# Kernel optimization log

Hardware: AMD Instinct MI355X
Metric: run time of the kernel (lower is better)

Reference implementation:

```python
import jax, jax.numpy as jnp
import numpy as np

B, T, H, V, O = 64, 2048, 8, 1000, 1000


def setup_inputs() -> dict:
    key = jax.random.key(0)
    ks = jax.random.split(key, 9)
    X = jax.random.randint(ks[0], (B, T), 0, V, dtype=jnp.int64)
    lengths = jax.random.randint(ks[1], (B,), 1, T + 1, dtype=jnp.int64)
    lengths = lengths.at[0].set(T)  # ensure max(lengths) == T (static output shape)
    s = 1.0 / np.sqrt(H)
    emb = jax.random.normal(ks[2], (V, H), dtype=jnp.float32)
    W_ih = jax.random.uniform(ks[3], (H, H), jnp.float32, -s, s)
    W_hh = jax.random.uniform(ks[4], (H, H), jnp.float32, -s, s)
    b_ih = jax.random.uniform(ks[5], (H,), jnp.float32, -s, s)
    b_hh = jax.random.uniform(ks[6], (H,), jnp.float32, -s, s)
    W_out = jax.random.uniform(ks[7], (O, H), jnp.float32, -s, s)
    b_out = jax.random.uniform(ks[8], (O,), jnp.float32, -s, s)
    return {"X": X, "lengths": lengths, "emb": emb, "W_ih": W_ih,
            "W_hh": W_hh, "b_ih": b_ih, "b_hh": b_hh,
            "W_out": W_out, "b_out": b_out}


def reference(X, lengths, emb, W_ih, W_hh, b_ih, b_hh, W_out, b_out):
    # Embedding gather: [B, T, H]
    x = emb[X]
    # Precompute input projection once (equivalent to per-step W_ih @ x_t)
    x_proj = jnp.einsum('bth,ih->bti', x, W_ih) + b_ih
    h0 = jnp.zeros((X.shape[0], W_hh.shape[0]), dtype=x.dtype)

    def step(h, xt):
        h = jnp.tanh(xt + h @ W_hh.T + b_hh)
        return h, h

    # scan over time: xs shape [T, B, H]
    _, hs = jax.lax.scan(step, h0, jnp.swapaxes(x_proj, 0, 1))
    out = jnp.swapaxes(hs, 0, 1)  # [B, T, H]
    # pad_packed_sequence semantics: positions >= length are zeroed before Linear
    t_idx = jnp.arange(out.shape[1])
    mask = (t_idx[None, :] < lengths[:, None]).astype(out.dtype)  # [B, T]
    out = out * mask[:, :, None]
    # Output projection: [B, T, O]
    logits = jnp.einsum('bth,oh->bto', out, W_out) + b_out
    return logits, lengths
```

## Files before the change

kernel.cpp:

```cpp
#include <hip/hip_runtime.h>
#include <cstdint>
#include <cstddef>

#define Bz 64
#define Tz 2048
#define Hz 8
#define Vz 1000
#define Oz 1000

typedef float f32x4 __attribute__((ext_vector_type(4)));

__global__ __launch_bounds__(256) void k_xproj(
    const int* __restrict__ X, const int* __restrict__ lengths,
    const float* __restrict__ emb, const float* __restrict__ W_ih,
    const float* __restrict__ b_ih, const float* __restrict__ b_hh,
    float* __restrict__ xpT, float* __restrict__ out_tail)
{
    int r = blockIdx.x * 256 + threadIdx.x;
    if (r < Bz * Tz) {
        int v = X[r];
        const float4* e4 = (const float4*)(emb + (size_t)v * Hz);
        float4 ea = e4[0], eb = e4[1];
        float res[8];
#pragma unroll
        for (int i = 0; i < 8; ++i) {
            const float* w = W_ih + i * 8;
            float a = b_ih[i] + b_hh[i];
            a = fmaf(ea.x, w[0], a); a = fmaf(ea.y, w[1], a);
            a = fmaf(ea.z, w[2], a); a = fmaf(ea.w, w[3], a);
            a = fmaf(eb.x, w[4], a); a = fmaf(eb.y, w[5], a);
            a = fmaf(eb.z, w[6], a); a = fmaf(eb.w, w[7], a);
            res[i] = a;
        }
        int b = r >> 11, t = r & 2047;
#pragma unroll
        for (int q = 0; q < 4; ++q) {
            *(float2*)(xpT + ((size_t)(b * 4 + q) * Tz + t) * 2) =
                make_float2(res[2 * q], res[2 * q + 1]);
        }
    }
    if (r < Bz) out_tail[r] = (float)lengths[r];
}

#define QROT(x, CTRL) \
    __int_as_float(__builtin_amdgcn_update_dpp(0, __float_as_int(x), (CTRL), 0xF, 0xF, true))

__device__ __forceinline__ float fast_tanh(float a) {
#if __has_builtin(__builtin_amdgcn_exp2f)
    float m = fminf(a * 2.885390081777927f, 126.0f);
    float e = __builtin_amdgcn_exp2f(m);
#else
    float m = fminf(a * 2.885390081777927f, 126.0f);
    float e = exp2f(m);
#endif
#if __has_builtin(__builtin_amdgcn_rcpf)
    return (e - 1.0f) * __builtin_amdgcn_rcpf(e + 1.0f);
#else
    return (e - 1.0f) / (e + 1.0f);
#endif
}

#define STEP(xx, yy, toff) do { \
    float p1x = QROT(h0, 0x39), p1y = QROT(h1, 0x39); \
    float p2x = QROT(h0, 0x4E), p2y = QROT(h1, 0x4E); \
    float p3x = QROT(h0, 0x93), p3y = QROT(h1, 0x93); \
    float a0 = fmaf(h0, w0[0], (xx)); \
    float a1 = fmaf(h0, w1[0], (yy)); \
    a0 = fmaf(h1,  w0[1], a0); a1 = fmaf(h1,  w1[1], a1); \
    a0 = fmaf(p1x, w0[2], a0); a1 = fmaf(p1x, w1[2], a1); \
    a0 = fmaf(p1y, w0[3], a0); a1 = fmaf(p1y, w1[3], a1); \
    a0 = fmaf(p2x, w0[4], a0); a1 = fmaf(p2x, w1[4], a1); \
    a0 = fmaf(p2y, w0[5], a0); a1 = fmaf(p2y, w1[5], a1); \
    a0 = fmaf(p3x, w0[6], a0); a1 = fmaf(p3x, w1[6], a1); \
    a0 = fmaf(p3y, w0[7], a0); a1 = fmaf(p3y, w1[7], a1); \
    h0 = fast_tanh(a0); h1 = fast_tanh(a1); \
    *(float2*)(hs_base + (size_t)(toff) * 8) = make_float2(h0, h1); \
} while (0)

__global__ __launch_bounds__(64) void k_scan(
    const float* __restrict__ xpT, const float* __restrict__ W_hh,
    float* __restrict__ hs)
{
    int lane = threadIdx.x;
    int b = blockIdx.x * 16 + (lane >> 2);
    int q = lane & 3;
    int i0 = 2 * q, i1 = 2 * q + 1;

    float w0[8], w1[8];
#pragma unroll
    for (int r = 0; r < 4; ++r) {
        int jj = ((q + r) & 3) * 2;
        w0[2 * r]     = W_hh[i0 * 8 + jj];
        w0[2 * r + 1] = W_hh[i0 * 8 + jj + 1];
        w1[2 * r]     = W_hh[i1 * 8 + jj];
        w1[2 * r + 1] = W_hh[i1 * 8 + jj + 1];
    }

    const float4* xp4 = (const float4*)(xpT + (size_t)(b * 4 + q) * Tz * 2);
    float* hs_base = hs + (size_t)b * Tz * 8 + 2 * q;

    float h0 = 0.0f, h1 = 0.0f;
    float4 c0 = xp4[0], c1 = xp4[1], c2 = xp4[2], c3 = xp4[3];

    for (int c = 0; c < Tz / 8; ++c) {
        float4 n0 = xp4[4 * c + 4], n1 = xp4[4 * c + 5];
        float4 n2 = xp4[4 * c + 6], n3 = xp4[4 * c + 7];
        int t0 = c * 8;
        STEP(c0.x, c0.y, t0 + 0); STEP(c0.z, c0.w, t0 + 1);
        STEP(c1.x, c1.y, t0 + 2); STEP(c1.z, c1.w, t0 + 3);
        STEP(c2.x, c2.y, t0 + 4); STEP(c2.z, c2.w, t0 + 5);
        STEP(c3.x, c3.y, t0 + 6); STEP(c3.z, c3.w, t0 + 7);
        c0 = n0; c1 = n1; c2 = n2; c3 = n3;
    }
}

__global__ __launch_bounds__(256) void k_out(
    const float* __restrict__ hs, const int* __restrict__ lengths,
    const float* __restrict__ W_out, const float* __restrict__ b_out,
    float* __restrict__ out)
{
    __shared__ float4 sh4[256];
    int tid = threadIdx.x;
    int r0 = blockIdx.x * 128;

    {
        int row = r0 + (tid >> 1);
        int b = row >> 11, t = row & 2047;
        float4 v = ((const float4*)hs)[(size_t)r0 * 2 + tid];
        if (t >= lengths[b]) v = make_float4(0.f, 0.f, 0.f, 0.f);
        sh4[tid] = v;
    }
    __syncthreads();

    if (tid >= Oz / 4) return;

    float w[4][8];
    float bo[4];
#pragma unroll
    for (int k = 0; k < 4; ++k) {
        const float4* wr = (const float4*)(W_out + (size_t)(tid * 4 + k) * 8);
        float4 wa = wr[0], wb = wr[1];
        w[k][0] = wa.x; w[k][1] = wa.y; w[k][2] = wa.z; w[k][3] = wa.w;
        w[k][4] = wb.x; w[k][5] = wb.y; w[k][6] = wb.z; w[k][7] = wb.w;
        bo[k] = b_out[tid * 4 + k];
    }

    for (int rr = 0; rr < 128; ++rr) {
        float4 ha = sh4[rr * 2], hb = sh4[rr * 2 + 1];
        float r[4];
#pragma unroll
        for (int k = 0; k < 4; ++k) {
            float a = bo[k];
            a = fmaf(ha.x, w[k][0], a); a = fmaf(ha.y, w[k][1], a);
            a = fmaf(ha.z, w[k][2], a); a = fmaf(ha.w, w[k][3], a);
            a = fmaf(hb.x, w[k][4], a); a = fmaf(hb.y, w[k][5], a);
            a = fmaf(hb.z, w[k][6], a); a = fmaf(hb.w, w[k][7], a);
            r[k] = a;
        }
        f32x4 acc = { r[0], r[1], r[2], r[3] };
        __builtin_nontemporal_store(
            acc, (f32x4*)(out + (size_t)(r0 + rr) * Oz) + tid);
    }
}

extern "C" void kernel_launch(void* const* d_in, const int* in_sizes, int n_in,
                              void* d_out, int out_size, void* d_ws, size_t ws_size,
                              hipStream_t stream)
{
    const int*   X       = (const int*)d_in[0];
    const int*   lengths = (const int*)d_in[1];
    const float* emb     = (const float*)d_in[2];
    const float* W_ih    = (const float*)d_in[3];
    const float* W_hh    = (const float*)d_in[4];
    const float* b_ih    = (const float*)d_in[5];
    const float* b_hh    = (const float*)d_in[6];
    const float* W_out   = (const float*)d_in[7];
    const float* b_out   = (const float*)d_in[8];

    float* out   = (float*)d_out;
    float* xpT   = (float*)d_ws;
    float* hs    = xpT + (size_t)Bz * Tz * Hz;

    float* out_tail = out + (size_t)Bz * Tz * Oz;

    k_xproj<<<(Bz * Tz + 255) / 256, 256, 0, stream>>>(X, lengths, emb, W_ih,
                                                       b_ih, b_hh, xpT, out_tail);
    k_scan<<<Bz / 16, 64, 0, stream>>>(xpT, W_hh, hs);
    k_out<<<(Bz * Tz) / 128, 256, 0, stream>>>(hs, lengths, W_out, b_out, out);
}
```

Baseline: 749.3 us.

## Fuse recurrent scan with output projection via progress-flag pipelining

Merges the scan and output-projection kernels into one persistent launch. Block 0 runs the recurrence across four waves and publishes per-wave progress counters. The other 255 blocks spin on those counters and project each 128-step chunk as soon as it is ready, so the large output write overlaps with the serial scan. It also folds the tanh exponent scale into the input projection and W_hh, and splits the FMA chain into a shallower tree to shorten the per-step dependency. The risks are spin-wait deadlock if block 0 is not scheduled, extra sync overhead, and the fused path depending on the workspace being large enough.

```diff
diff --git a/kernel.cpp b/kernel.cpp
--- a/kernel.cpp
+++ b/kernel.cpp
@@ -8,13 +8,17 @@
 #define Vz 1000
 #define Oz 1000
 
+#define SCALE 2.885390081777927f
+
 typedef float f32x4 __attribute__((ext_vector_type(4)));
+typedef float f32x2 __attribute__((ext_vector_type(2)));
 
 __global__ __launch_bounds__(256) void k_xproj(
     const int* __restrict__ X, const int* __restrict__ lengths,
     const float* __restrict__ emb, const float* __restrict__ W_ih,
     const float* __restrict__ b_ih, const float* __restrict__ b_hh,
-    float* __restrict__ xpT, float* __restrict__ out_tail)
+    float* __restrict__ xpT, float* __restrict__ out_tail,
+    int* __restrict__ prog)
 {
     int r = blockIdx.x * 256 + threadIdx.x;
     if (r < Bz * Tz) {
@@ -30,7 +34,7 @@
             a = fmaf(ea.z, w[2], a); a = fmaf(ea.w, w[3], a);
             a = fmaf(eb.x, w[4], a); a = fmaf(eb.y, w[5], a);
             a = fmaf(eb.z, w[6], a); a = fmaf(eb.w, w[7], a);
-            res[i] = a;
+            res[i] = a * SCALE;
         }
         int b = r >> 11, t = r & 2047;
 #pragma unroll
@@ -40,17 +44,17 @@
         }
     }
     if (r < Bz) out_tail[r] = (float)lengths[r];
+    if (prog != nullptr && r < 4) prog[r] = 0;
 }
 
 #define QROT(x, CTRL) \
     __int_as_float(__builtin_amdgcn_update_dpp(0, __float_as_int(x), (CTRL), 0xF, 0xF, true))
 
-__device__ __forceinline__ float fast_tanh(float a) {
+__device__ __forceinline__ float fast_tanh_pre(float m) {
+    m = fminf(m, 126.0f);
 #if __has_builtin(__builtin_amdgcn_exp2f)
-    float m = fminf(a * 2.885390081777927f, 126.0f);
     float e = __builtin_amdgcn_exp2f(m);
 #else
-    float m = fminf(a * 2.885390081777927f, 126.0f);
     float e = exp2f(m);
 #endif
 #if __has_builtin(__builtin_amdgcn_rcpf)
@@ -64,36 +68,33 @@
     float p1x = QROT(h0, 0x39), p1y = QROT(h1, 0x39); \
     float p2x = QROT(h0, 0x4E), p2y = QROT(h1, 0x4E); \
     float p3x = QROT(h0, 0x93), p3y = QROT(h1, 0x93); \
-    float a0 = fmaf(h0, w0[0], (xx)); \
-    float a1 = fmaf(h0, w1[0], (yy)); \
-    a0 = fmaf(h1,  w0[1], a0); a1 = fmaf(h1,  w1[1], a1); \
-    a0 = fmaf(p1x, w0[2], a0); a1 = fmaf(p1x, w1[2], a1); \
-    a0 = fmaf(p1y, w0[3], a0); a1 = fmaf(p1y, w1[3], a1); \
-    a0 = fmaf(p2x, w0[4], a0); a1 = fmaf(p2x, w1[4], a1); \
-    a0 = fmaf(p2y, w0[5], a0); a1 = fmaf(p2y, w1[5], a1); \
-    a0 = fmaf(p3x, w0[6], a0); a1 = fmaf(p3x, w1[6], a1); \
-    a0 = fmaf(p3y, w0[7], a0); a1 = fmaf(p3y, w1[7], a1); \
-    h0 = fast_tanh(a0); h1 = fast_tanh(a1); \
-    *(float2*)(hs_base + (size_t)(toff) * 8) = make_float2(h0, h1); \
+    float s0a = fmaf(h1, w0[1], fmaf(h0, w0[0], (xx))); \
+    float s0b = fmaf(h1, w1[1], fmaf(h0, w1[0], (yy))); \
+    float s1a = fmaf(p1y, w0[3], p1x * w0[2]); \
+    float s1b = fmaf(p1y, w1[3], p1x * w1[2]); \
+    float s2a = fmaf(p2y, w0[5], p2x * w0[4]); \
+    float s2b = fmaf(p2y, w1[5], p2x * w1[4]); \
+    float s3a = fmaf(p3y, w0[7], p3x * w0[6]); \
+    float s3b = fmaf(p3y, w1[7], p3x * w1[6]); \
+    h0 = fast_tanh_pre((s0a + s1a) + (s2a + s3a)); \
+    h1 = fast_tanh_pre((s0b + s1b) + (s2b + s3b)); \
+    f32x2 hv = { h0, h1 }; \
+    __builtin_nontemporal_store(hv, (f32x2*)(hs_base + (size_t)(toff) * 8)); \
 } while (0)
 
-__global__ __launch_bounds__(64) void k_scan(
+__device__ __forceinline__ void scan_run(
     const float* __restrict__ xpT, const float* __restrict__ W_hh,
-    float* __restrict__ hs)
-{
-    int lane = threadIdx.x;
-    int b = blockIdx.x * 16 + (lane >> 2);
-    int q = lane & 3;
+    float* __restrict__ hs, int b, int q, int* prog, int wv)
+{
     int i0 = 2 * q, i1 = 2 * q + 1;
-
     float w0[8], w1[8];
 #pragma unroll
     for (int r = 0; r < 4; ++r) {
         int jj = ((q + r) & 3) * 2;
-        w0[2 * r]     = W_hh[i0 * 8 + jj];
-        w0[2 * r + 1] = W_hh[i0 * 8 + jj + 1];
-        w1[2 * r]     = W_hh[i1 * 8 + jj];
-        w1[2 * r + 1] = W_hh[i1 * 8 + jj + 1];
+        w0[2 * r]     = W_hh[i0 * 8 + jj]     * SCALE;
+        w0[2 * r + 1] = W_hh[i0 * 8 + jj + 1] * SCALE;
+        w1[2 * r]     = W_hh[i1 * 8 + jj]     * SCALE;
+        w1[2 * r + 1] = W_hh[i1 * 8 + jj + 1] * SCALE;
     }
 
     const float4* xp4 = (const float4*)(xpT + (size_t)(b * 4 + q) * Tz * 2);
@@ -102,15 +103,98 @@
     float h0 = 0.0f, h1 = 0.0f;
     float4 c0 = xp4[0], c1 = xp4[1], c2 = xp4[2], c3 = xp4[3];
 
-    for (int c = 0; c < Tz / 8; ++c) {
-        float4 n0 = xp4[4 * c + 4], n1 = xp4[4 * c + 5];
-        float4 n2 = xp4[4 * c + 6], n3 = xp4[4 * c + 7];
-        int t0 = c * 8;
+    for (int g = 0; g < Tz / 8; ++g) {
+        float4 n0 = xp4[4 * g + 4], n1 = xp4[4 * g + 5];
+        float4 n2 = xp4[4 * g + 6], n3 = xp4[4 * g + 7];
+        int t0 = g * 8;
         STEP(c0.x, c0.y, t0 + 0); STEP(c0.z, c0.w, t0 + 1);
         STEP(c1.x, c1.y, t0 + 2); STEP(c1.z, c1.w, t0 + 3);
         STEP(c2.x, c2.y, t0 + 4); STEP(c2.z, c2.w, t0 + 5);
         STEP(c3.x, c3.y, t0 + 6); STEP(c3.z, c3.w, t0 + 7);
         c0 = n0; c1 = n1; c2 = n2; c3 = n3;
+        if (prog != nullptr && (g & 15) == 15) {
+            if ((threadIdx.x & 63) == 0)
+                __hip_atomic_store(&prog[wv], (g >> 4) + 1,
+                                   __ATOMIC_RELEASE, __HIP_MEMORY_SCOPE_AGENT);
+        }
+    }
+}
+
+__global__ __launch_bounds__(64) void k_scan(
+    const float* __restrict__ xpT, const float* __restrict__ W_hh,
+    float* __restrict__ hs)
+{
+    int lane = threadIdx.x;
+    scan_run(xpT, W_hh, hs, blockIdx.x * 16 + (lane >> 2), lane & 3, nullptr, 0);
+}
+
+__global__ __launch_bounds__(256) void k_fused(
+    const float* __restrict__ xpT, const float* __restrict__ W_hh,
+    float* __restrict__ hs, const int* __restrict__ lengths,
+    const float* __restrict__ W_out, const float* __restrict__ b_out,
+    float* __restrict__ out, int* __restrict__ prog)
+{
+    __shared__ float4 sh4[256];
+    int tid = threadIdx.x;
+
+    if (blockIdx.x == 0) {
+        int lane = tid & 63, wv = tid >> 6;
+        scan_run(xpT, W_hh, hs, wv * 16 + (lane >> 2), lane & 3, prog, wv);
+        return;
+    }
+
+    int k0 = blockIdx.x - 1;
+
+    float w[4][8], bo[4];
+    if (tid < Oz / 4) {
+#pragma unroll
+        for (int k = 0; k < 4; ++k) {
+            const float4* wr = (const float4*)(W_out + (size_t)(tid * 4 + k) * 8);
+            float4 wa = wr[0], wb = wr[1];
+            w[k][0] = wa.x; w[k][1] = wa.y; w[k][2] = wa.z; w[k][3] = wa.w;
+            w[k][4] = wb.x; w[k][5] = wb.y; w[k][6] = wb.z; w[k][7] = wb.w;
+            bo[k] = b_out[tid * 4 + k];
+        }
+    }
+
+    for (int tau = k0; tau < (Bz * Tz) / 128; tau += 255) {
+        int c = tau >> 6;
+        int b = tau & 63;
+        if (tid == 0) {
+            while (__hip_atomic_load(&prog[b >> 4], __ATOMIC_ACQUIRE,
+                                     __HIP_MEMORY_SCOPE_AGENT) <= c)
+                __builtin_amdgcn_s_sleep(8);
+        }
+        __syncthreads();
+
+        int r0 = b * Tz + c * 128;
+        {
+            int t = c * 128 + (tid >> 1);
+            float4 v = ((const float4*)hs)[(size_t)r0 * 2 + tid];
+            if (t >= lengths[b]) v = make_float4(0.f, 0.f, 0.f, 0.f);
+            sh4[tid] = v;
+        }
+        __syncthreads();
+
+        if (tid < Oz / 4) {
+            for (int rr = 0; rr < 128; ++rr) {
+                float4 ha = sh4[rr * 2], hb = sh4[rr * 2 + 1];
+                float r[4];
+#pragma unroll
+                for (int k = 0; k < 4; ++k) {
+                    float a = bo[k];
+                    a = fmaf(ha.x, w[k][0], a); a = fmaf(ha.y, w[k][1], a);
+                    a = fmaf(ha.z, w[k][2], a); a = fmaf(ha.w, w[k][3], a);
+                    a = fmaf(hb.x, w[k][4], a); a = fmaf(hb.y, w[k][5], a);
+                    a = fmaf(hb.z, w[k][6], a); a = fmaf(hb.w, w[k][7], a);
+                    r[k] = a;
+                }
+                f32x4 acc = { r[0], r[1], r[2], r[3] };
+                __builtin_nontemporal_store(
+                    acc, (f32x4*)(out + (size_t)(r0 + rr) * Oz) + tid);
+            }
+        }
+        __syncthreads();
     }
 }
 
@@ -183,8 +267,18 @@
 
     float* out_tail = out + (size_t)Bz * Tz * Oz;
 
+    size_t base = (size_t)Bz * Tz * Hz * 4 * 2;
+    bool fused = (ws_size >= base + 64);
+    int* prog = fused ? (int*)((char*)d_ws + base) : nullptr;
+
     k_xproj<<<(Bz * Tz + 255) / 256, 256, 0, stream>>>(X, lengths, emb, W_ih,
-                                                       b_ih, b_hh, xpT, out_tail);
-    k_scan<<<Bz / 16, 64, 0, stream>>>(xpT, W_hh, hs);
-    k_out<<<(Bz * Tz) / 128, 256, 0, stream>>>(hs, lengths, W_out, b_out, out);
-}
+                                                       b_ih, b_hh, xpT, out_tail,
+                                                       prog);
+    if (fused) {
+        k_fused<<<256, 256, 0, stream>>>(xpT, W_hh, hs, lengths, W_out, b_out,
+                                         out, prog);
+    } else {
+        k_scan<<<Bz / 16, 64, 0, stream>>>(xpT, W_hh, hs);
+        k_out<<<(Bz * Tz) / 128, 256, 0, stream>>>(hs, lengths, W_out, b_out, out);
+    }
+}
```

Measured after the change: 2.218 ms. 2.96x slower.

## Fold tanh scale into weights, tree-reduce recurrence, store hidden states time-major

Applied to the files above, without the earlier changes.

Pre-multiplies the input projection and W_hh by the 2/ln2 tanh scale, so the serial scan step skips a multiply and a min. It also splits the 8-term dot product into independent partial sums to shorten the dependent FMA chain on the critical path. Hidden states are now stored time-major, so each k_out block handles two timesteps across all batches, which changes the output write pattern to rows spread across batches. The clamp now applies only to the input-projection part rather than the full pre-activation, so very large recurrent contributions could behave slightly differently, although W_hh bounds make this unlikely.

```diff
diff --git a/kernel.cpp b/kernel.cpp
--- a/kernel.cpp
+++ b/kernel.cpp
@@ -7,6 +7,9 @@
 #define Hz 8
 #define Vz 1000
 #define Oz 1000
+
+#define SCALE 2.885390081777927f
+#define XPCLAMP 117.0f
 
 typedef float f32x4 __attribute__((ext_vector_type(4)));
 
@@ -30,7 +33,7 @@
             a = fmaf(ea.z, w[2], a); a = fmaf(ea.w, w[3], a);
             a = fmaf(eb.x, w[4], a); a = fmaf(eb.y, w[5], a);
             a = fmaf(eb.z, w[6], a); a = fmaf(eb.w, w[7], a);
-            res[i] = a;
+            res[i] = fminf(a * SCALE, XPCLAMP);
         }
         int b = r >> 11, t = r & 2047;
 #pragma unroll
@@ -45,12 +48,10 @@
 #define QROT(x, CTRL) \
     __int_as_float(__builtin_amdgcn_update_dpp(0, __float_as_int(x), (CTRL), 0xF, 0xF, true))
 
-__device__ __forceinline__ float fast_tanh(float a) {
+__device__ __forceinline__ float fast_tanh_pre(float m) {
 #if __has_builtin(__builtin_amdgcn_exp2f)
-    float m = fminf(a * 2.885390081777927f, 126.0f);
     float e = __builtin_amdgcn_exp2f(m);
 #else
-    float m = fminf(a * 2.885390081777927f, 126.0f);
     float e = exp2f(m);
 #endif
 #if __has_builtin(__builtin_amdgcn_rcpf)
@@ -64,17 +65,17 @@
     float p1x = QROT(h0, 0x39), p1y = QROT(h1, 0x39); \
     float p2x = QROT(h0, 0x4E), p2y = QROT(h1, 0x4E); \
     float p3x = QROT(h0, 0x93), p3y = QROT(h1, 0x93); \
-    float a0 = fmaf(h0, w0[0], (xx)); \
-    float a1 = fmaf(h0, w1[0], (yy)); \
-    a0 = fmaf(h1,  w0[1], a0); a1 = fmaf(h1,  w1[1], a1); \
-    a0 = fmaf(p1x, w0[2], a0); a1 = fmaf(p1x, w1[2], a1); \
-    a0 = fmaf(p1y, w0[3], a0); a1 = fmaf(p1y, w1[3], a1); \
-    a0 = fmaf(p2x, w0[4], a0); a1 = fmaf(p2x, w1[4], a1); \
-    a0 = fmaf(p2y, w0[5], a0); a1 = fmaf(p2y, w1[5], a1); \
-    a0 = fmaf(p3x, w0[6], a0); a1 = fmaf(p3x, w1[6], a1); \
-    a0 = fmaf(p3y, w0[7], a0); a1 = fmaf(p3y, w1[7], a1); \
-    h0 = fast_tanh(a0); h1 = fast_tanh(a1); \
-    *(float2*)(hs_base + (size_t)(toff) * 8) = make_float2(h0, h1); \
+    float s0a = fmaf(h1, w0[1], fmaf(h0, w0[0], (xx))); \
+    float s0b = fmaf(h1, w1[1], fmaf(h0, w1[0], (yy))); \
+    float s1a = fmaf(p1y, w0[3], p1x * w0[2]); \
+    float s1b = fmaf(p1y, w1[3], p1x * w1[2]); \
+    float s2a = fmaf(p2y, w0[5], p2x * w0[4]); \
+    float s2b = fmaf(p2y, w1[5], p2x * w1[4]); \
+    float s3a = fmaf(p3y, w0[7], p3x * w0[6]); \
+    float s3b = fmaf(p3y, w1[7], p3x * w1[6]); \
+    h0 = fast_tanh_pre((s0a + s1a) + (s2a + s3a)); \
+    h1 = fast_tanh_pre((s0b + s1b) + (s2b + s3b)); \
+    *(float2*)(hs_base + (size_t)(toff) * (Bz * Hz)) = make_float2(h0, h1); \
 } while (0)
 
 __global__ __launch_bounds__(64) void k_scan(
@@ -90,14 +91,14 @@
 #pragma unroll
     for (int r = 0; r < 4; ++r) {
         int jj = ((q + r) & 3) * 2;
-        w0[2 * r]     = W_hh[i0 * 8 + jj];
-        w0[2 * r + 1] = W_hh[i0 * 8 + jj + 1];
-        w1[2 * r]     = W_hh[i1 * 8 + jj];
-        w1[2 * r + 1] = W_hh[i1 * 8 + jj + 1];
+        w0[2 * r]     = W_hh[i0 * 8 + jj]     * SCALE;
+        w0[2 * r + 1] = W_hh[i0 * 8 + jj + 1] * SCALE;
+        w1[2 * r]     = W_hh[i1 * 8 + jj]     * SCALE;
+        w1[2 * r + 1] = W_hh[i1 * 8 + jj + 1] * SCALE;
     }
 
     const float4* xp4 = (const float4*)(xpT + (size_t)(b * 4 + q) * Tz * 2);
-    float* hs_base = hs + (size_t)b * Tz * 8 + 2 * q;
+    float* hs_base = hs + (size_t)b * Hz + 2 * q;
 
     float h0 = 0.0f, h1 = 0.0f;
     float4 c0 = xp4[0], c1 = xp4[1], c2 = xp4[2], c3 = xp4[3];
@@ -121,13 +122,12 @@
 {
     __shared__ float4 sh4[256];
     int tid = threadIdx.x;
-    int r0 = blockIdx.x * 128;
+    int t0 = blockIdx.x * 2;
 
     {
-        int row = r0 + (tid >> 1);
-        int b = row >> 11, t = row & 2047;
-        float4 v = ((const float4*)hs)[(size_t)r0 * 2 + tid];
-        if (t >= lengths[b]) v = make_float4(0.f, 0.f, 0.f, 0.f);
+        float4 v = ((const float4*)hs)[(size_t)t0 * 128 + tid];
+        int tt = tid >> 7, b = (tid & 127) >> 1;
+        if (t0 + tt >= lengths[b]) v = make_float4(0.f, 0.f, 0.f, 0.f);
         sh4[tid] = v;
     }
     __syncthreads();
@@ -147,6 +147,7 @@
 
     for (int rr = 0; rr < 128; ++rr) {
         float4 ha = sh4[rr * 2], hb = sh4[rr * 2 + 1];
+        int tt = rr >> 6, b = rr & 63;
         float r[4];
 #pragma unroll
         for (int k = 0; k < 4; ++k) {
@@ -159,7 +160,7 @@
         }
         f32x4 acc = { r[0], r[1], r[2], r[3] };
         __builtin_nontemporal_store(
-            acc, (f32x4*)(out + (size_t)(r0 + rr) * Oz) + tid);
+            acc, (f32x4*)(out + ((size_t)b * Tz + t0 + tt) * Oz) + tid);
     }
 }
 
@@ -186,5 +187,5 @@
     k_xproj<<<(Bz * Tz + 255) / 256, 256, 0, stream>>>(X, lengths, emb, W_ih,
                                                        b_ih, b_hh, xpT, out_tail);
     k_scan<<<Bz / 16, 64, 0, stream>>>(xpT, W_hh, hs);
-    k_out<<<(Bz * Tz) / 128, 256, 0, stream>>>(hs, lengths, W_out, b_out, out);
+    k_out<<<Tz / 2, 256, 0, stream>>>(hs, lengths, W_out, b_out, out);
 }
```

After: 735.9 us. About the same (-1.8%).
